# Optimization experiments

Hardware: AMD Instinct MI355X
Metric: run time of the kernel (lower is better)

The kernel has to match this reference:

```python
import jax, jax.numpy as jnp
import numpy as np

H, W = 128, 128  # image_shape


def setup_inputs() -> dict:
    key = jax.random.key(0)
    Y = jax.random.uniform(key, (32, H * W), dtype=jnp.float32)
    return {"Y": Y}


def reference(Y):
    # Binarize and reshape to images: [B, H, W]
    Yb = (Y > 0.5).astype(jnp.float32).reshape(-1, H, W)

    # DP over rows: heights[i, j] = number of consecutive 1s ending at row i in column j
    def step(h, row):
        h = (h + 1.0) * row
        return h, h

    _, heights = jax.lax.scan(step, jnp.zeros((Yb.shape[0], W), Yb.dtype),
                              jnp.swapaxes(Yb, 0, 1))
    heights = jnp.swapaxes(heights, 0, 1)  # [B, H, W]

    # Largest rectangle in histogram, vectorized over all rows.
    # For bar j: left[j] = prev index k with h[k] < h[j] (else -1),
    #            right[j] = next index k with h[k] < h[j] (else W).
    # This matches the monotonic-stack scan (pops while h[stack[-1]] >= h[i]).
    idx = jnp.arange(W)
    kk = idx[:, None]  # candidate index k (axis -2)
    jj = idx[None, :]  # bar index j (axis -1)
    less = heights[..., :, None] < heights[..., None, :]  # [B, H, W, W]; less[k, j] = h[k] < h[j]
    left = jnp.max(jnp.where(less & (kk < jj), kk, -1), axis=-2)   # [B, H, W]
    right = jnp.min(jnp.where(less & (kk > jj), kk, W), axis=-2)   # [B, H, W]

    area = heights * (right - left - 1).astype(heights.dtype)  # [B, H, W]
    maxarea = jnp.max(area, axis=(1, 2))  # [B]; all-zero image -> 0, matching original
    return maxarea.astype(jnp.int32)[:, None]  # [B, 1]
```

## Files before the change

kernel.cpp:

```cpp
#include <hip/hip_runtime.h>

static constexpr int H = 128;
static constexpr int W = 128;
static constexpr int B = 32;
static constexpr int RPB = 4;
static constexpr int WIN = RPB + 31;
static constexpr int GPB = H / RPB;

__global__ __launch_bounds__(W) void lr_rows(const float* __restrict__ Y,
                                             int* __restrict__ partials,
                                             int* __restrict__ out,
                                             int use_atomic) {
    const int blk = blockIdx.x;
    const int b = blk >> 5;
    const int rg = blk & (GPB - 1);
    const int r_top = rg * RPB + (RPB - 1);
    const int j = threadIdx.x;
    const int wid = j >> 6;
    const int lane = j & 63;
    const float* __restrict__ ycol = Y + (size_t)b * H * W + j;

    unsigned long long mask = 0ULL;
    #pragma unroll
    for (int k = 0; k < WIN; ++k) {
        int t = r_top - k; t = t < 0 ? 0 : t;
        if (ycol[(size_t)t * W] > 0.5f) mask |= (1ULL << k);
    }
    if (r_top < WIN - 1) mask &= (2ULL << r_top) - 1ULL;

    int h[RPB];
    #pragma unroll
    for (int s = 0; s < RPB; ++s) {
        const int row = r_top - s;
        int hs = __builtin_ctzll(~(mask >> s));
        if (hs == WIN - s && row - hs >= 0) {
            int t = row - hs;
            while (t >= 0 && ycol[(size_t)t * W] > 0.5f) { ++hs; --t; }
        }
        h[s] = hs;
    }

    __shared__ unsigned long long tbl[RPB][H + 1][2];
    __shared__ int hmx[RPB][2];
    __shared__ int wmax[2];

    #pragma unroll
    for (int s = 0; s < RPB; ++s) {
        int hm = h[s];
        #pragma unroll
        for (int off = 32; off > 0; off >>= 1)
            hm = max(hm, __shfl_xor(hm, off, 64));
        if (lane == 0) hmx[s][wid] = hm;
    }
    __syncthreads();

    #pragma unroll
    for (int s = 0; s < RPB; ++s) {
        const int hmax = max(hmx[s][0], hmx[s][1]);
        for (int t = 1; t <= hmax; ++t) {
            const unsigned long long m = __ballot(h[s] < t);
            if (lane == 0) tbl[s][t][wid] = m;
        }
    }
    __syncthreads();

    int acc = 0;
    #pragma unroll
    for (int s = 0; s < RPB; ++s) {
        const unsigned long long mlo = tbl[s][h[s]][0];
        const unsigned long long mhi = tbl[s][h[s]][1];
        int left, right;
        if (j < 64) {
            const unsigned long long below = mlo & ((1ULL << j) - 1ULL);
            const unsigned long long above = mlo & ~((2ULL << j) - 1ULL);
            left  = below ? 63 - __builtin_clzll(below) : -1;
            right = above ? __builtin_ctzll(above)
                          : (mhi ? 64 + __builtin_ctzll(mhi) : W);
        } else {
            const int jj = j - 64;
            const unsigned long long below = mhi & ((1ULL << jj) - 1ULL);
            const unsigned long long above = mhi & ~((2ULL << jj) - 1ULL);
            left  = below ? 127 - __builtin_clzll(below)
                          : (mlo ? 63 - __builtin_clzll(mlo) : -1);
            right = above ? 64 + __builtin_ctzll(above) : W;
        }
        acc = max(acc, h[s] * (right - left - 1));
    }

    #pragma unroll
    for (int off = 32; off > 0; off >>= 1)
        acc = max(acc, __shfl_xor(acc, off, 64));
    if (lane == 0) wmax[wid] = acc;
    __syncthreads();
    if (j == 0) {
        const int m = max(wmax[0], wmax[1]);
        if (use_atomic) atomicMax(&out[b], m);
        else partials[blk] = m;
    }
}

__global__ __launch_bounds__(64) void lr_reduce(const int* __restrict__ partials,
                                                int* __restrict__ out) {
    const int b = blockIdx.x;
    const int j = threadIdx.x;
    int v = (j < GPB) ? partials[b * GPB + j] : 0;
    #pragma unroll
    for (int off = 32; off > 0; off >>= 1)
        v = max(v, __shfl_xor(v, off, 64));
    if (j == 0) out[b] = v;
}

extern "C" void kernel_launch(void* const* d_in, const int* in_sizes, int n_in,
                              void* d_out, int out_size, void* d_ws, size_t ws_size,
                              hipStream_t stream) {
    const float* Y = (const float*)d_in[0];
    int* out = (int*)d_out;

    if (ws_size >= (size_t)(B * GPB) * sizeof(int)) {
        int* partials = (int*)d_ws;
        lr_rows<<<B * GPB, W, 0, stream>>>(Y, partials, out, 0);
        lr_reduce<<<B, 64, 0, stream>>>(partials, out);
    } else {
        hipMemsetAsync(out, 0, (size_t)out_size * sizeof(int), stream);
        lr_rows<<<B * GPB, W, 0, stream>>>(Y, nullptr, out, 1);
    }
}
```

Before: 14.22 us.

## Use single-wavefront blocks handling two columns per lane, drop shared-memory table

Each block now uses one 64-lane wavefront, and every lane handles two columns (j and j+64). All cross-column communication happens through ballots kept in registers, so the shared-memory ballot table, the per-wave maxima and the __syncthreads barriers are gone. The ballot loop is fused across the RPB rows and runs up to the overall max height. Each lane keeps the two ballot masks for its own height. This trades half the threads per block and more register pressure and ballot work per lane for no LDS traffic and no block-level synchronisation.

Measured after the change: 13.10 us (median of 2 runs). 1.09x faster.

```diff
diff --git a/kernel.cpp b/kernel.cpp
--- a/kernel.cpp
+++ b/kernel.cpp
@@ -7,95 +7,93 @@
 static constexpr int WIN = RPB + 31;
 static constexpr int GPB = H / RPB;
 
-__global__ __launch_bounds__(W) void lr_rows(const float* __restrict__ Y,
-                                             int* __restrict__ partials,
-                                             int* __restrict__ out,
-                                             int use_atomic) {
+__global__ __launch_bounds__(64) void lr_rows(const float* __restrict__ Y,
+                                              int* __restrict__ partials,
+                                              int* __restrict__ out,
+                                              int use_atomic) {
     const int blk = blockIdx.x;
     const int b = blk >> 5;
     const int rg = blk & (GPB - 1);
     const int r_top = rg * RPB + (RPB - 1);
-    const int j = threadIdx.x;
-    const int wid = j >> 6;
-    const int lane = j & 63;
-    const float* __restrict__ ycol = Y + (size_t)b * H * W + j;
+    const int l = threadIdx.x;
+    const float* __restrict__ yA = Y + (size_t)b * H * W + l;
+    const float* __restrict__ yB = yA + 64;
 
-    unsigned long long mask = 0ULL;
+    unsigned long long mA = 0ULL, mB = 0ULL;
     #pragma unroll
     for (int k = 0; k < WIN; ++k) {
         int t = r_top - k; t = t < 0 ? 0 : t;
-        if (ycol[(size_t)t * W] > 0.5f) mask |= (1ULL << k);
+        if (yA[(size_t)t * W] > 0.5f) mA |= (1ULL << k);
+        if (yB[(size_t)t * W] > 0.5f) mB |= (1ULL << k);
     }
-    if (r_top < WIN - 1) mask &= (2ULL << r_top) - 1ULL;
+    if (r_top < WIN - 1) {
+        const unsigned long long keep = (2ULL << r_top) - 1ULL;
+        mA &= keep; mB &= keep;
+    }
 
-    int h[RPB];
+    int hA[RPB], hB[RPB];
     #pragma unroll
     for (int s = 0; s < RPB; ++s) {
-        const int row = r_top - s;
-        int hs = __builtin_ctzll(~(mask >> s));
-        if (hs == WIN - s && row - hs >= 0) {
-            int t = row - hs;
-            while (t >= 0 && ycol[(size_t)t * W] > 0.5f) { ++hs; --t; }
+        const int r = r_top - s;
+        int a = __builtin_ctzll(~(mA >> s));
+        if (a == WIN - s && r - a >= 0) {
+            int t = r - a;
+            while (t >= 0 && yA[(size_t)t * W] > 0.5f) { ++a; --t; }
         }
-        h[s] = hs;
+        int c = __builtin_ctzll(~(mB >> s));
+        if (c == WIN - s && r - c >= 0) {
+            int t = r - c;
+            while (t >= 0 && yB[(size_t)t * W] > 0.5f) { ++c; --t; }
+        }
+        hA[s] = a; hB[s] = c;
     }
 
-    __shared__ unsigned long long tbl[RPB][H + 1][2];
-    __shared__ int hmx[RPB][2];
-    __shared__ int wmax[2];
+    int hm = 0;
+    #pragma unroll
+    for (int s = 0; s < RPB; ++s) hm = max(hm, max(hA[s], hB[s]));
+    #pragma unroll
+    for (int off = 32; off > 0; off >>= 1)
+        hm = max(hm, __shfl_xor(hm, off, 64));
 
-    #pragma unroll
-    for (int s = 0; s < RPB; ++s) {
-        int hm = h[s];
+    unsigned long long loA[RPB] = {}, hiA[RPB] = {};
+    unsigned long long loB[RPB] = {}, hiB[RPB] = {};
+    for (int t = 1; t <= hm; ++t) {
         #pragma unroll
-        for (int off = 32; off > 0; off >>= 1)
-            hm = max(hm, __shfl_xor(hm, off, 64));
-        if (lane == 0) hmx[s][wid] = hm;
-    }
-    __syncthreads();
-
-    #pragma unroll
-    for (int s = 0; s < RPB; ++s) {
-        const int hmax = max(hmx[s][0], hmx[s][1]);
-        for (int t = 1; t <= hmax; ++t) {
-            const unsigned long long m = __ballot(h[s] < t);
-            if (lane == 0) tbl[s][t][wid] = m;
+        for (int s = 0; s < RPB; ++s) {
+            const unsigned long long lo = __ballot(hA[s] < t);
+            const unsigned long long hi = __ballot(hB[s] < t);
+            if (hA[s] == t) { loA[s] = lo; hiA[s] = hi; }
+            if (hB[s] == t) { loB[s] = lo; hiB[s] = hi; }
         }
     }
-    __syncthreads();
 
     int acc = 0;
     #pragma unroll
     for (int s = 0; s < RPB; ++s) {
-        const unsigned long long mlo = tbl[s][h[s]][0];
-        const unsigned long long mhi = tbl[s][h[s]][1];
-        int left, right;
-        if (j < 64) {
-            const unsigned long long below = mlo & ((1ULL << j) - 1ULL);
-            const unsigned long long above = mlo & ~((2ULL << j) - 1ULL);
-            left  = below ? 63 - __builtin_clzll(below) : -1;
-            right = above ? __builtin_ctzll(above)
-                          : (mhi ? 64 + __builtin_ctzll(mhi) : W);
-        } else {
-            const int jj = j - 64;
-            const unsigned long long below = mhi & ((1ULL << jj) - 1ULL);
-            const unsigned long long above = mhi & ~((2ULL << jj) - 1ULL);
-            left  = below ? 127 - __builtin_clzll(below)
-                          : (mlo ? 63 - __builtin_clzll(mlo) : -1);
-            right = above ? 64 + __builtin_ctzll(above) : W;
+        {
+            const unsigned long long below = loA[s] & ((1ULL << l) - 1ULL);
+            const unsigned long long above = loA[s] & ~((2ULL << l) - 1ULL);
+            const int left  = below ? 63 - __builtin_clzll(below) : -1;
+            const int right = above ? __builtin_ctzll(above)
+                                    : (hiA[s] ? 64 + __builtin_ctzll(hiA[s]) : W);
+            acc = max(acc, hA[s] * (right - left - 1));
         }
-        acc = max(acc, h[s] * (right - left - 1));
+        {
+            const unsigned long long below = hiB[s] & ((1ULL << l) - 1ULL);
+            const unsigned long long above = hiB[s] & ~((2ULL << l) - 1ULL);
+            const int left  = below ? 64 + 63 - __builtin_clzll(below)
+                                    : (loB[s] ? 63 - __builtin_clzll(loB[s]) : -1);
+            const int right = above ? 64 + __builtin_ctzll(above) : W;
+            acc = max(acc, hB[s] * (right - left - 1));
+        }
     }
 
     #pragma unroll
     for (int off = 32; off > 0; off >>= 1)
         acc = max(acc, __shfl_xor(acc, off, 64));
-    if (lane == 0) wmax[wid] = acc;
-    __syncthreads();
-    if (j == 0) {
-        const int m = max(wmax[0], wmax[1]);
-        if (use_atomic) atomicMax(&out[b], m);
-        else partials[blk] = m;
+    if (l == 0) {
+        if (use_atomic) atomicMax(&out[b], acc);
+        else partials[blk] = acc;
     }
 }
 
@@ -118,10 +116,10 @@
 
     if (ws_size >= (size_t)(B * GPB) * sizeof(int)) {
         int* partials = (int*)d_ws;
-        lr_rows<<<B * GPB, W, 0, stream>>>(Y, partials, out, 0);
+        lr_rows<<<B * GPB, 64, 0, stream>>>(Y, partials, out, 0);
         lr_reduce<<<B, 64, 0, stream>>>(partials, out);
     } else {
         hipMemsetAsync(out, 0, (size_t)out_size * sizeof(int), stream);
-        lr_rows<<<B * GPB, W, 0, stream>>>(Y, nullptr, out, 1);
+        lr_rows<<<B * GPB, 64, 0, stream>>>(Y, nullptr, out, 1);
     }
 }
```
